# Kernel optimization log

Hardware: AMD Instinct MI355X
Metric: run time of the kernel (lower is better)

The kernel has to match this reference:

```python
import jax, jax.numpy as jnp
import numpy as np

N_NODES = 100000
N_EDGES = 1600000
F_IN = 128
N_HEADS = 4
F_OUT = 32
NEG_SLOPE = 0.2


def setup_inputs() -> dict:
    key = jax.random.key(0)
    k_feat, k_src, k_dst, k_w, k_as, k_ad, k_res = jax.random.split(key, 7)
    feat = jax.random.normal(k_feat, (N_NODES, F_IN), dtype=jnp.float32)
    src = jax.random.randint(k_src, (N_EDGES,), 0, N_NODES, dtype=jnp.int32)
    dst = jax.random.randint(k_dst, (N_EDGES,), 0, N_NODES, dtype=jnp.int32)
    s = 1.0 / np.sqrt(F_IN)
    W = jax.random.normal(k_w, (F_IN, N_HEADS * F_OUT), dtype=jnp.float32) * s
    att_src = jax.random.normal(k_as, (N_HEADS, F_OUT), dtype=jnp.float32) * 0.1
    att_dst = jax.random.normal(k_ad, (N_HEADS, F_OUT), dtype=jnp.float32) * 0.1
    W_res = jax.random.normal(k_res, (F_IN, N_HEADS * F_OUT), dtype=jnp.float32) * s
    return {"feat": feat, "W": W, "att_src": att_src, "att_dst": att_dst,
            "W_res": W_res, "src": src, "dst": dst}


def reference(feat, W, att_src, att_dst, W_res, src, dst):
    N = feat.shape[0]
    H, Fo = att_src.shape
    # shared linear projection (GATConv, bias=False): [N, H, Fo]
    x = (feat @ W).reshape(N, H, Fo)
    # per-node attention logits: [N, H]
    a_s = jnp.einsum('nhf,hf->nh', x, att_src)
    a_d = jnp.einsum('nhf,hf->nh', x, att_dst)
    # edge-wise scores + LeakyReLU: [E, H]
    e = jax.nn.leaky_relu(a_s[src] + a_d[dst], negative_slope=NEG_SLOPE)
    # segment softmax over incoming edges of each dst node
    e_max = jax.ops.segment_max(e, dst, num_segments=N)  # [N, H]
    e_exp = jnp.exp(e - e_max[dst])                       # [E, H]
    denom = jax.ops.segment_sum(e_exp, dst, num_segments=N)  # [N, H]
    alpha = e_exp / denom[dst]                            # [E, H]
    # weighted scatter-add aggregation: [N, H, Fo]
    msg = x[src] * alpha[:, :, None]
    out = jax.ops.segment_sum(msg, dst, num_segments=N)
    # residual projection
    res = (feat @ W_res).reshape(N, H, Fo)
    return out + res
```

## Files before the change

kernel.cpp:

```cpp
#include <hip/hip_runtime.h>
#include <math.h>

#define NN 100000
#define NE 1600000
#define F_IN 128
#define C 128
#define NEG_SLOPE 0.2f
#define PROJ_NB ((NN + 63) / 64)

#define NBLK1 256
#define EPB ((NE + NBLK1 - 1) / NBLK1)
#define BSHIFT 9
#define NBUCK ((NN + 511) / 512)

typedef __attribute__((ext_vector_type(8))) short short8;
typedef __attribute__((ext_vector_type(4))) float f32x4;
typedef __attribute__((ext_vector_type(4))) float floatx4;
typedef __attribute__((ext_vector_type(4))) unsigned short ushortx4;

static __device__ __forceinline__ unsigned short f2bf(float f) {
    unsigned int u = __float_as_uint(f);
    unsigned int r = (u + 0x7fff + ((u >> 16) & 1)) >> 16;
    return (unsigned short)r;
}
static __device__ __forceinline__ float bf2f(unsigned short h) {
    return __uint_as_float((unsigned int)h << 16);
}

__global__ __launch_bounds__(256)
void wconv_kernel(const float* __restrict__ W,
                  const float* __restrict__ Wr,
                  unsigned short* __restrict__ Btf)
{
    int g = blockIdx.x * 256 + threadIdx.x;
    int nt = g >> 8;
    int kc = (g >> 6) & 3;
    int l  = g & 63;
    int n  = nt * 16 + (l & 15);
    int kb = kc * 32 + (l >> 4) * 8;
    unsigned short v[8];
    #pragma unroll
    for (int j = 0; j < 8; ++j) {
        int k = kb + j;
        float f = (n < 128) ? W[(size_t)k * 128 + n] : Wr[(size_t)k * 128 + (n - 128)];
        v[j] = f2bf(f);
    }
    *(short8*)&Btf[(size_t)g * 8] = *(short8*)v;
}

__global__ __launch_bounds__(256, 4)
void proj_kernel(const float* __restrict__ feat,
                 const unsigned short* __restrict__ Btf,
                 const float* __restrict__ att_src,
                 const float* __restrict__ att_dst,
                 unsigned short* __restrict__ xb,
                 unsigned short* __restrict__ resb,
                 float* __restrict__ a_s,
                 float* __restrict__ a_d)
{
    __shared__ __align__(16) float T2all[4][16 * 68];
    __shared__ float s_as[64][4];
    __shared__ float s_ad[64][4];
    const int tid = threadIdx.x;

    const int base = blockIdx.x * 64;
    const int l = tid & 63;
    const int w = tid >> 6;
    const int quad = l >> 4;
    const int lo16 = l & 15;
    const int arow = w * 16 + lo16;
    const int nclamp = min(base + arow, NN - 1);

    short8 af[4];
    #pragma unroll
    for (int kc = 0; kc < 4; ++kc) {
        const float* fp = &feat[(size_t)nclamp * F_IN + kc * 32 + quad * 8];
        floatx4 f0 = __builtin_nontemporal_load((const floatx4*)fp);
        floatx4 f1 = __builtin_nontemporal_load((const floatx4*)(fp + 4));
        unsigned short v[8];
        v[0] = f2bf(f0.x); v[1] = f2bf(f0.y); v[2] = f2bf(f0.z); v[3] = f2bf(f0.w);
        v[4] = f2bf(f1.x); v[5] = f2bf(f1.y); v[6] = f2bf(f1.z); v[7] = f2bf(f1.w);
        af[kc] = *(short8*)v;
    }

    f32x4 acc[16];
    #pragma unroll
    for (int nt = 0; nt < 16; ++nt) acc[nt] = (f32x4){0.f, 0.f, 0.f, 0.f};

    #pragma unroll
    for (int nt = 0; nt < 16; ++nt) {
        const unsigned short* bp = &Btf[(size_t)(nt * 4) * 512 + l * 8];
        short8 b0 = *(const short8*)&bp[0];
        short8 b1 = *(const short8*)&bp[512];
        short8 b2 = *(const short8*)&bp[1024];
        short8 b3 = *(const short8*)&bp[1536];
        acc[nt] = __builtin_amdgcn_mfma_f32_16x16x32_bf16(af[0], b0, acc[nt], 0, 0, 0);
        acc[nt] = __builtin_amdgcn_mfma_f32_16x16x32_bf16(af[1], b1, acc[nt], 0, 0, 0);
        acc[nt] = __builtin_amdgcn_mfma_f32_16x16x32_bf16(af[2], b2, acc[nt], 0, 0, 0);
        acc[nt] = __builtin_amdgcn_mfma_f32_16x16x32_bf16(af[3], b3, acc[nt], 0, 0, 0);
    }

    float* T2 = T2all[w];
    const int g  = l >> 4;
    const int cf = (l & 15) * 4;

    #pragma unroll
    for (int p = 0; p < 2; ++p) {
        #pragma unroll
        for (int ntl = 0; ntl < 4; ++ntl) {
            int nt = p * 4 + ntl;
            #pragma unroll
            for (int r = 0; r < 4; ++r)
                T2[(quad * 4 + r) * 68 + ntl * 16 + lo16] = acc[nt][r];
        }
        floatx4 ws4 = *(const floatx4*)&att_src[p * 64 + cf];
        floatx4 wd4 = *(const floatx4*)&att_dst[p * 64 + cf];
        float ps[4], pd[4];
        #pragma unroll
        for (int it = 0; it < 4; ++it) {
            int row = it * 4 + g;
            floatx4 v = *(floatx4*)&T2[row * 68 + cf];
            int node = base + w * 16 + row;
            ushortx4 hh;
            hh.x = f2bf(v.x); hh.y = f2bf(v.y); hh.z = f2bf(v.z); hh.w = f2bf(v.w);
            if (node < NN)
                __builtin_nontemporal_store(hh,
                    (ushortx4*)&xb[(size_t)node * C + p * 64 + cf]);
            ps[it] = v.x * ws4.x + v.y * ws4.y + v.z * ws4.z + v.w * ws4.w;
            pd[it] = v.x * wd4.x + v.y * wd4.y + v.z * wd4.z + v.w * wd4.w;
        }
        #pragma unroll
        for (int it = 0; it < 4; ++it) {
            #pragma unroll
            for (int d = 1; d < 8; d <<= 1) {
                ps[it] += __shfl_xor(ps[it], d, 64);
                pd[it] += __shfl_xor(pd[it], d, 64);
            }
        }
        if ((l & 7) == 0) {
            int hh = p * 2 + ((l & 15) >> 3);
            #pragma unroll
            for (int it = 0; it < 4; ++it) {
                int lr = w * 16 + it * 4 + g;
                s_as[lr][hh] = ps[it];
                s_ad[lr][hh] = pd[it];
            }
        }
    }

    #pragma unroll
    for (int p = 0; p < 2; ++p) {
        #pragma unroll
        for (int ntl = 0; ntl < 4; ++ntl) {
            int nt = 8 + p * 4 + ntl;
            #pragma unroll
            for (int r = 0; r < 4; ++r)
                T2[(quad * 4 + r) * 68 + ntl * 16 + lo16] = acc[nt][r];
        }
        #pragma unroll
        for (int it = 0; it < 4; ++it) {
            int row = it * 4 + g;
            floatx4 v = *(floatx4*)&T2[row * 68 + cf];
            int node = base + w * 16 + row;
            ushortx4 hh;
            hh.x = f2bf(v.x); hh.y = f2bf(v.y); hh.z = f2bf(v.z); hh.w = f2bf(v.w);
            if (node < NN)
                __builtin_nontemporal_store(hh,
                    (ushortx4*)&resb[(size_t)node * C + p * 64 + cf]);
        }
    }

    __syncthreads();
    int idx = blockIdx.x * 256 + tid;
    if (idx < NN * 4) {
        a_s[idx] = ((float*)s_as)[tid];
        a_d[idx] = ((float*)s_ad)[tid];
    }
}

__global__ __launch_bounds__(256)
void sort1_kernel(const int* __restrict__ dst, int* __restrict__ counts)
{
    __shared__ int h[256];
    const int tid = threadIdx.x;
    h[tid] = 0;
    __syncthreads();
    const int e0 = blockIdx.x * EPB;
    const int e1 = min(NE, e0 + EPB);
    for (int e = e0 + tid; e < e1; e += 256)
        atomicAdd(&h[dst[e] >> BSHIFT], 1);
    __syncthreads();
    counts[blockIdx.x * 256 + tid] = h[tid];
}

__global__ __launch_bounds__(256)
void sortscan_kernel(int* __restrict__ counts, int* __restrict__ bucket_base)
{
    __shared__ int wsum[4];
    const int t = threadIdx.x, lane = t & 63, wid = t >> 6;
    int run = 0;
    for (int b = 0; b < NBLK1; ++b) {
        int v = counts[b * 256 + t];
        counts[b * 256 + t] = run;
        run += v;
    }
    int v0 = run, v = run;
    #pragma unroll
    for (int off = 1; off < 64; off <<= 1) {
        int u = __shfl_up(v, off, 64);
        if (lane >= off) v += u;
    }
    if (lane == 63) wsum[wid] = v;
    __syncthreads();
    if (t == 0) {
        int r = 0;
        #pragma unroll
        for (int s = 0; s < 4; ++s) { int tmp = wsum[s]; wsum[s] = r; r += tmp; }
    }
    __syncthreads();
    int excl = wsum[wid] + (v - v0);
    bucket_base[t] = excl;
    if (t == 255) bucket_base[256] = excl + v0;
}

__global__ __launch_bounds__(256)
void sort2_kernel(const int* __restrict__ src, const int* __restrict__ dst,
                  const int* __restrict__ counts,
                  const int* __restrict__ bucket_base,
                  int* __restrict__ bpack)
{
    __shared__ int cur[256];
    const int tid = threadIdx.x;
    cur[tid] = bucket_base[tid] + counts[blockIdx.x * 256 + tid];
    __syncthreads();
    const int e0 = blockIdx.x * EPB;
    const int e1 = min(NE, e0 + EPB);
    for (int e = e0 + tid; e < e1; e += 256) {
        int d = dst[e];
        int s = src[e];
        int pos = atomicAdd(&cur[d >> BSHIFT], 1);
        bpack[pos] = ((d & 511) << 20) | s;
    }
}

__global__ __launch_bounds__(512)
void sort3_kernel(const int* __restrict__ bpack,
                  const int* __restrict__ bucket_base,
                  int* __restrict__ row_ptr,
                  int* __restrict__ csr_src)
{
    __shared__ int cnt[512];
    __shared__ int cur[512];
    __shared__ int wsum[8];
    const int t = threadIdx.x, lane = t & 63, wid = t >> 6;
    const int b = blockIdx.x;
    const int ebeg = bucket_base[b];
    const int eend = bucket_base[b + 1];
    cnt[t] = 0;
    __syncthreads();
    for (int e = ebeg + t; e < eend; e += 512)
        atomicAdd(&cnt[bpack[e] >> 20], 1);
    __syncthreads();
    int v0 = cnt[t], v = v0;
    #pragma unroll
    for (int off = 1; off < 64; off <<= 1) {
        int u = __shfl_up(v, off, 64);
        if (lane >= off) v += u;
    }
    if (lane == 63) wsum[wid] = v;
    __syncthreads();
    if (t == 0) {
        int r = 0;
        #pragma unroll
        for (int s = 0; s < 8; ++s) { int tmp = wsum[s]; wsum[s] = r; r += tmp; }
    }
    __syncthreads();
    int excl = wsum[wid] + (v - v0);
    cur[t] = excl;
    int n = (b << BSHIFT) + t;
    if (n < NN) row_ptr[n] = ebeg + excl;
    if (b == NBUCK - 1 && t == 0) row_ptr[NN] = NE;
    __syncthreads();
    for (int e = ebeg + t; e < eend; e += 512) {
        int p = bpack[e];
        int pos = atomicAdd(&cur[p >> 20], 1);
        csr_src[ebeg + pos] = p & 0xFFFFF;
    }
}

__global__ __launch_bounds__(256)
void agg_kernel(const unsigned short* __restrict__ xb,
                const unsigned short* __restrict__ resb,
                const float* __restrict__ a_s,
                const float* __restrict__ a_d,
                const int* __restrict__ row_ptr,
                const int* __restrict__ csr_src,
                float* __restrict__ out)
{
    __shared__ float s_alpha[4][64 * 4];
    __shared__ int   s_srcs[4][64];
    const int tid = threadIdx.x;
    const int w = tid >> 6;
    const int l = tid & 63;
    const int n = blockIdx.x * 4 + w;
    if (n >= NN) return;
    const int r0  = row_ptr[n];
    const int deg = row_ptr[n + 1] - r0;

    const int half = l >> 5;
    const int hl   = l & 31;
    const int h    = hl >> 3;

    if (deg == 0) {
        if (half == 0) {
            ushort4 rv = *(const ushort4*)&resb[(size_t)n * C + hl * 4];
            floatx4 o;
            o.x = bf2f(rv.x); o.y = bf2f(rv.y);
            o.z = bf2f(rv.z); o.w = bf2f(rv.w);
            __builtin_nontemporal_store(o, (floatx4*)&out[(size_t)n * C + hl * 4]);
        }
        return;
    }

    const float4 ad4 = *(const float4*)&a_d[n * 4];

    float ax = 0.f, ay = 0.f, az = 0.f, aw = 0.f;
    float dx = 0.f, dy = 0.f, dz = 0.f, dw = 0.f;

    for (int c0 = 0; c0 < deg; c0 += 64) {
        int e = c0 + l;
        int s = 0;
        float4 ex = {0.f, 0.f, 0.f, 0.f};
        if (e < deg) {
            s = csr_src[r0 + e];
            float4 as4 = *(const float4*)&a_s[s * 4];
            float e0 = as4.x + ad4.x, e1 = as4.y + ad4.y;
            float e2 = as4.z + ad4.z, e3 = as4.w + ad4.w;
            e0 = (e0 > 0.f) ? e0 : NEG_SLOPE * e0;
            e1 = (e1 > 0.f) ? e1 : NEG_SLOPE * e1;
            e2 = (e2 > 0.f) ? e2 : NEG_SLOPE * e2;
            e3 = (e3 > 0.f) ? e3 : NEG_SLOPE * e3;
            ex.x = __expf(e0); ex.y = __expf(e1);
            ex.z = __expf(e2); ex.w = __expf(e3);
            dx += ex.x; dy += ex.y; dz += ex.z; dw += ex.w;
        }
        s_srcs[w][l] = s;
        *(float4*)&s_alpha[w][l * 4] = ex;

        int cn = min(64, deg - c0);
        int iters = (cn + 1) >> 1;
        #pragma unroll 2
        for (int i = 0; i < iters; ++i) {
            int ii = i * 2 + half;
            int   si = s_srcs[w][ii];
            float al = s_alpha[w][ii * 4 + h];
            ushort4 uv = *(const ushort4*)&xb[(size_t)si * C + hl * 4];
            ax = fmaf(al, bf2f(uv.x), ax);
            ay = fmaf(al, bf2f(uv.y), ay);
            az = fmaf(al, bf2f(uv.z), az);
            aw = fmaf(al, bf2f(uv.w), aw);
        }
    }

    #pragma unroll
    for (int d = 32; d > 0; d >>= 1) {
        dx += __shfl_xor(dx, d, 64);
        dy += __shfl_xor(dy, d, 64);
        dz += __shfl_xor(dz, d, 64);
        dw += __shfl_xor(dw, d, 64);
    }
    float den = (h == 0) ? dx : (h == 1) ? dy : (h == 2) ? dz : dw;
    float inv = 1.f / den;

    ax += __shfl_xor(ax, 32, 64);
    ay += __shfl_xor(ay, 32, 64);
    az += __shfl_xor(az, 32, 64);
    aw += __shfl_xor(aw, 32, 64);

    if (half == 0) {
        ushort4 rv = *(const ushort4*)&resb[(size_t)n * C + hl * 4];
        floatx4 o;
        o.x = bf2f(rv.x) + ax * inv;
        o.y = bf2f(rv.y) + ay * inv;
        o.z = bf2f(rv.z) + az * inv;
        o.w = bf2f(rv.w) + aw * inv;
        __builtin_nontemporal_store(o, (floatx4*)&out[(size_t)n * C + hl * 4]);
    }
}

extern "C" void kernel_launch(void* const* d_in, const int* in_sizes, int n_in,
                              void* d_out, int out_size, void* d_ws, size_t ws_size,
                              hipStream_t stream)
{
    const float* feat    = (const float*)d_in[0];
    const float* W       = (const float*)d_in[1];
    const float* att_src = (const float*)d_in[2];
    const float* att_dst = (const float*)d_in[3];
    const float* W_res   = (const float*)d_in[4];
    const int*   src     = (const int*)d_in[5];
    const int*   dst     = (const int*)d_in[6];
    float* out = (float*)d_out;

    char* p = (char*)d_ws;
    unsigned short* xb   = (unsigned short*)p; p += (size_t)NN * C * sizeof(unsigned short);
    unsigned short* resb = (unsigned short*)p; p += (size_t)NN * C * sizeof(unsigned short);
    unsigned short* Btf  = (unsigned short*)p; p += (size_t)256 * 128 * sizeof(unsigned short);
    float* a_s = (float*)p;            p += (size_t)NN * 4 * sizeof(float);
    float* a_d = (float*)p;            p += (size_t)NN * 4 * sizeof(float);
    int* row_ptr = (int*)p;            p += (size_t)(NN + 1) * sizeof(int);
    int* counts  = (int*)p;            p += (size_t)NBLK1 * 256 * sizeof(int);
    int* bucket_base = (int*)p;        p += (size_t)257 * sizeof(int);
    int* bpack   = (int*)p;            p += (size_t)NE * sizeof(int);
    int* csr_src = (int*)p;            p += (size_t)NE * sizeof(int);

    wconv_kernel<<<16, 256, 0, stream>>>(W, W_res, Btf);
    proj_kernel<<<PROJ_NB, 256, 0, stream>>>(
        feat, Btf, att_src, att_dst, xb, resb, a_s, a_d);
    sort1_kernel<<<NBLK1, 256, 0, stream>>>(dst, counts);
    sortscan_kernel<<<1, 256, 0, stream>>>(counts, bucket_base);
    sort2_kernel<<<NBLK1, 256, 0, stream>>>(src, dst, counts, bucket_base, bpack);
    sort3_kernel<<<NBUCK, 512, 0, stream>>>(bpack, bucket_base, row_ptr, csr_src);
    agg_kernel<<<(NN + 3) / 4, 256, 0, stream>>>(xb, resb, a_s, a_d, row_ptr, csr_src, out);
}
```

Measured before the change: 267.7 us.

## Map four destination nodes per wavefront in aggregation with 16-byte gathers

After: 264.9 us. No clear change (-1.0%).

```diff
diff --git a/kernel.cpp b/kernel.cpp
--- a/kernel.cpp
+++ b/kernel.cpp
@@ -199,6 +199,7 @@
     __shared__ int wsum[4];
     const int t = threadIdx.x, lane = t & 63, wid = t >> 6;
     int run = 0;
+    #pragma unroll 8
     for (int b = 0; b < NBLK1; ++b) {
         int v = counts[b * 256 + t];
         counts[b * 256 + t] = run;
@@ -297,38 +298,33 @@
                 const int* __restrict__ csr_src,
                 float* __restrict__ out)
 {
-    __shared__ float s_alpha[4][64 * 4];
-    __shared__ int   s_srcs[4][64];
+    __shared__ float s_alpha[4][4][68];
+    __shared__ int   s_srcs[4][4][17];
     const int tid = threadIdx.x;
-    const int w = tid >> 6;
-    const int l = tid & 63;
-    const int n = blockIdx.x * 4 + w;
-    if (n >= NN) return;
+    const int w   = tid >> 6;
+    const int l   = tid & 63;
+    const int q   = l >> 4;
+    const int t16 = l & 15;
+    const int h   = t16 >> 2;
+
+    const int n = blockIdx.x * 16 + w * 4 + q;
     const int r0  = row_ptr[n];
     const int deg = row_ptr[n + 1] - r0;
 
-    const int half = l >> 5;
-    const int hl   = l & 31;
-    const int h    = hl >> 3;
-
-    if (deg == 0) {
-        if (half == 0) {
-            ushort4 rv = *(const ushort4*)&resb[(size_t)n * C + hl * 4];
-            floatx4 o;
-            o.x = bf2f(rv.x); o.y = bf2f(rv.y);
-            o.z = bf2f(rv.z); o.w = bf2f(rv.w);
-            __builtin_nontemporal_store(o, (floatx4*)&out[(size_t)n * C + hl * 4]);
-        }
-        return;
-    }
-
+    short8 rv = *(const short8*)&resb[(size_t)n * C + t16 * 8];
     const float4 ad4 = *(const float4*)&a_d[n * 4];
 
-    float ax = 0.f, ay = 0.f, az = 0.f, aw = 0.f;
+    int dm = deg;
+    dm = max(dm, __shfl_xor(dm, 16, 64));
+    dm = max(dm, __shfl_xor(dm, 32, 64));
+
+    float acc8[8];
+    #pragma unroll
+    for (int j = 0; j < 8; ++j) acc8[j] = 0.f;
     float dx = 0.f, dy = 0.f, dz = 0.f, dw = 0.f;
 
-    for (int c0 = 0; c0 < deg; c0 += 64) {
-        int e = c0 + l;
+    for (int c0 = 0; c0 < dm; c0 += 16) {
+        int e = c0 + t16;
         int s = 0;
         float4 ex = {0.f, 0.f, 0.f, 0.f};
         if (e < deg) {
@@ -344,48 +340,47 @@
             ex.z = __expf(e2); ex.w = __expf(e3);
             dx += ex.x; dy += ex.y; dz += ex.z; dw += ex.w;
         }
-        s_srcs[w][l] = s;
-        *(float4*)&s_alpha[w][l * 4] = ex;
-
-        int cn = min(64, deg - c0);
-        int iters = (cn + 1) >> 1;
+        s_srcs[w][q][t16] = s;
+        *(float4*)&s_alpha[w][q][t16 * 4] = ex;
+
+        int cn = min(16, deg - c0);
         #pragma unroll 2
-        for (int i = 0; i < iters; ++i) {
-            int ii = i * 2 + half;
-            int   si = s_srcs[w][ii];
-            float al = s_alpha[w][ii * 4 + h];
-            ushort4 uv = *(const ushort4*)&xb[(size_t)si * C + hl * 4];
-            ax = fmaf(al, bf2f(uv.x), ax);
-            ay = fmaf(al, bf2f(uv.y), ay);
-            az = fmaf(al, bf2f(uv.z), az);
-            aw = fmaf(al, bf2f(uv.w), aw);
-        }
-    }
-
-    #pragma unroll
-    for (int d = 32; d > 0; d >>= 1) {
+        for (int i = 0; i < cn; ++i) {
+            int   si = s_srcs[w][q][i];
+            float al = s_alpha[w][q][i * 4 + h];
+            short8 uv = *(const short8*)&xb[(size_t)si * C + t16 * 8];
+            acc8[0] = fmaf(al, bf2f((unsigned short)uv[0]), acc8[0]);
+            acc8[1] = fmaf(al, bf2f((unsigned short)uv[1]), acc8[1]);
+            acc8[2] = fmaf(al, bf2f((unsigned short)uv[2]), acc8[2]);
+            acc8[3] = fmaf(al, bf2f((unsigned short)uv[3]), acc8[3]);
+            acc8[4] = fmaf(al, bf2f((unsigned short)uv[4]), acc8[4]);
+            acc8[5] = fmaf(al, bf2f((unsigned short)uv[5]), acc8[5]);
+            acc8[6] = fmaf(al, bf2f((unsigned short)uv[6]), acc8[6]);
+            acc8[7] = fmaf(al, bf2f((unsigned short)uv[7]), acc8[7]);
+        }
+    }
+
+    #pragma unroll
+    for (int d = 1; d < 16; d <<= 1) {
         dx += __shfl_xor(dx, d, 64);
         dy += __shfl_xor(dy, d, 64);
         dz += __shfl_xor(dz, d, 64);
         dw += __shfl_xor(dw, d, 64);
     }
     float den = (h == 0) ? dx : (h == 1) ? dy : (h == 2) ? dz : dw;
-    float inv = 1.f / den;
-
-    ax += __shfl_xor(ax, 32, 64);
-    ay += __shfl_xor(ay, 32, 64);
-    az += __shfl_xor(az, 32, 64);
-    aw += __shfl_xor(aw, 32, 64);
-
-    if (half == 0) {
-        ushort4 rv = *(const ushort4*)&resb[(size_t)n * C + hl * 4];
-        floatx4 o;
-        o.x = bf2f(rv.x) + ax * inv;
-        o.y = bf2f(rv.y) + ay * inv;
-        o.z = bf2f(rv.z) + az * inv;
-        o.w = bf2f(rv.w) + aw * inv;
-        __builtin_nontemporal_store(o, (floatx4*)&out[(size_t)n * C + hl * 4]);
-    }
+    float inv = (deg > 0) ? 1.f / den : 0.f;
+
+    floatx4 o0, o1;
+    o0.x = bf2f((unsigned short)rv[0]) + acc8[0] * inv;
+    o0.y = bf2f((unsigned short)rv[1]) + acc8[1] * inv;
+    o0.z = bf2f((unsigned short)rv[2]) + acc8[2] * inv;
+    o0.w = bf2f((unsigned short)rv[3]) + acc8[3] * inv;
+    o1.x = bf2f((unsigned short)rv[4]) + acc8[4] * inv;
+    o1.y = bf2f((unsigned short)rv[5]) + acc8[5] * inv;
+    o1.z = bf2f((unsigned short)rv[6]) + acc8[6] * inv;
+    o1.w = bf2f((unsigned short)rv[7]) + acc8[7] * inv;
+    __builtin_nontemporal_store(o0, (floatx4*)&out[(size_t)n * C + t16 * 8]);
+    __builtin_nontemporal_store(o1, (floatx4*)&out[(size_t)n * C + t16 * 8 + 4]);
 }
 
 extern "C" void kernel_launch(void* const* d_in, const int* in_sizes, int n_in,
@@ -420,5 +415,5 @@
     sortscan_kernel<<<1, 256, 0, stream>>>(counts, bucket_base);
     sort2_kernel<<<NBLK1, 256, 0, stream>>>(src, dst, counts, bucket_base, bpack);
     sort3_kernel<<<NBUCK, 512, 0, stream>>>(bpack, bucket_base, row_ptr, csr_src);
-    agg_kernel<<<(NN + 3) / 4, 256, 0, stream>>>(xb, resb, a_s, a_d, row_ptr, csr_src, out);
-}
+    agg_kernel<<<NN / 16, 256, 0, stream>>>(xb, resb, a_s, a_d, row_ptr, csr_src, out);
+}
```
